# Kernel tuning notes

Measured on AMD Instinct MI355X. Metric: run time of the kernel, lower is better.

## Reference

```python
import jax, jax.numpy as jnp
import numpy as np

V, D, H, L, S_MAX = 32000, 1024, 16, 4, 1024
HD = D // H          # head dim = 64
FF = 4 * D           # mlp hidden = 4096
B, S = 2, 1024


def _layernorm(x, w, b, eps=1e-5):
    mu = jnp.mean(x, axis=-1, keepdims=True)
    var = jnp.mean(jnp.square(x - mu), axis=-1, keepdims=True)
    return (x - mu) * jax.lax.rsqrt(var + eps) * w + b


def setup_inputs() -> dict:
    key = jax.random.key(0)
    ks = jax.random.split(key, 16)
    r = lambda k, shape: (jax.random.normal(k, shape, dtype=jnp.float32) * 0.02)
    return {
        "input_ids": jax.random.randint(ks[0], (B, S), 0, V),
        "tok_emb": r(ks[1], (V, D)),
        "pos_emb": r(ks[2], (S_MAX, D)),
        "ln1_w": jnp.ones((L, D)), "ln1_b": jnp.zeros((L, D)),
        "ln2_w": jnp.ones((L, D)), "ln2_b": jnp.zeros((L, D)),
        "q_w": r(ks[3], (L, D, D)), "q_b": jnp.zeros((L, D)),
        "k_w": r(ks[4], (L, D, D)), "k_b": jnp.zeros((L, D)),
        "v_w": r(ks[5], (L, D, D)), "v_b": jnp.zeros((L, D)),
        "o_w": r(ks[6], (L, D, D)), "o_b": jnp.zeros((L, D)),
        "fc1_w": r(ks[7], (L, FF, D)), "fc1_b": jnp.zeros((L, FF)),
        "fc2_w": r(ks[8], (L, D, FF)), "fc2_b": jnp.zeros((L, D)),
        "lnf_w": jnp.ones((D,)), "lnf_b": jnp.zeros((D,)),
        "head_w": r(ks[9], (V, D)),
    }


def reference(input_ids, tok_emb, pos_emb, ln1_w, ln1_b, ln2_w, ln2_b,
              q_w, q_b, k_w, k_b, v_w, v_b, o_w, o_b,
              fc1_w, fc1_b, fc2_w, fc2_b, lnf_w, lnf_b, head_w):
    b, s = input_ids.shape
    x = tok_emb[input_ids] + pos_emb[:s][None, :, :]          # [B,S,D]
    causal = jnp.tril(jnp.ones((s, s), dtype=bool))           # [S,S]
    scale = 1.0 / np.sqrt(HD)
    for i in range(L):
        # --- causal MHA block ---
        h = _layernorm(x, ln1_w[i], ln1_b[i])
        q = (h @ q_w[i].T + q_b[i]).reshape(b, s, H, HD)
        k = (h @ k_w[i].T + k_b[i]).reshape(b, s, H, HD)
        v = (h @ v_w[i].T + v_b[i]).reshape(b, s, H, HD)
        scores = jnp.einsum('bqhd,bkhd->bhqk', q, k) * scale  # [B,H,S,S]
        scores = jnp.where(causal[None, None], scores, -jnp.inf)
        attn = jax.nn.softmax(scores, axis=-1)
        y = jnp.einsum('bhqk,bkhd->bqhd', attn, v).reshape(b, s, D)
        x = x + (y @ o_w[i].T + o_b[i])
        # --- GELU MLP block (exact gelu, matching torch F.gelu default) ---
        h = _layernorm(x, ln2_w[i], ln2_b[i])
        h = jax.nn.gelu(h @ fc1_w[i].T + fc1_b[i], approximate=False)
        x = x + (h @ fc2_w[i].T + fc2_b[i])
    x = _layernorm(x, lnf_w, lnf_b)
    logits = x[:, -1, :] @ head_w.T                           # [B,V]
    return logits
```

## Files before the change

### kernel.cpp

```cpp
#include <hip/hip_runtime.h>

#define V_SIZE 32000
#define D_DIM  1024
#define H_HEADS 16
#define L_LAYERS 4
#define HD_DIM 64
#define FF_DIM 4096
#define B_BATCH 2
#define S_SEQ  1024
#define M_ROWS (B_BATCH*S_SEQ)
#define KSPL   2

typedef short  s16x8 __attribute__((ext_vector_type(8)));
typedef unsigned short u16x8 __attribute__((ext_vector_type(8)));
typedef float  f32x4 __attribute__((ext_vector_type(4)));
typedef unsigned short u16;
typedef unsigned int   u32;

__device__ inline u16 f2bf(float f){
    u32 u = __float_as_uint(f);
    return (u16)((u + 0x7FFFu + ((u >> 16) & 1u)) >> 16);
}
__device__ inline float b2f(u32 v){ return __uint_as_float(v << 16); }

__device__ inline float gelu_f(float v){
    float y = 0.7978845608f * (v + 0.044715f*v*v*v);
    y = fmaxf(-15.f, fminf(15.f, y));
    float u = __expf(-2.f*y);
    return v / (1.f + u);
}

__device__ inline char* lds_swz(void* base, int row, int byteoff){
    return (char*)base + row*128 + (byteoff ^ ((row & 7) << 4));
}

__device__ inline void gload16(const u16* g, u16* l){
    __builtin_amdgcn_global_load_lds(
        (const __attribute__((address_space(1))) void*)g,
        (__attribute__((address_space(3))) void*)l, 16, 0, 0);
}

__device__ inline int swz_src_col(int lin){
    int row = lin >> 3, s8 = lin & 7;
    return (s8*8) ^ ((row & 7) << 3);
}

__global__ __launch_bounds__(256) void cvt_all_k(
    const float* __restrict__ qw, const float* __restrict__ kw,
    const float* __restrict__ vw, const float* __restrict__ ow,
    const float* __restrict__ f1w, const float* __restrict__ f2w,
    u16* __restrict__ w_qkv, u16* __restrict__ w_o,
    u16* __restrict__ w_f1, u16* __restrict__ w_f2)
{
    const long M1 = 1L << 20;
    const int bx = blockIdx.x;
    const float* s; u16* d; long base;
    if (bx < 3072){
        int which = bx >> 10;
        s = (which==0) ? qw : ((which==1) ? kw : vw);
        base = (long)(bx & 1023) * 4096;
        long layer = base >> 20, rem = base & (M1 - 1);
        d = w_qkv + layer*3*M1 + which*M1 + rem;
        s += base;
    } else if (bx < 4096){
        base = (long)(bx - 3072) * 4096; s = ow  + base; d = w_o  + base;
    } else if (bx < 8192){
        base = (long)(bx - 4096) * 4096; s = f1w + base; d = w_f1 + base;
    } else {
        base = (long)(bx - 8192) * 4096; s = f2w + base; d = w_f2 + base;
    }
    const int t4 = threadIdx.x * 4;
#pragma unroll
    for (int j = 0; j < 4; j++){
        float4 v = *(const float4*)(s + j*1024 + t4);
        uint2 pk;
        pk.x = (u32)f2bf(v.x) | ((u32)f2bf(v.y) << 16);
        pk.y = (u32)f2bf(v.z) | ((u32)f2bf(v.w) << 16);
        *(uint2*)(d + j*1024 + t4) = pk;
    }
}

__global__ __launch_bounds__(256) void embed_ln_k(
    const int* __restrict__ ids, const float* __restrict__ tok,
    const float* __restrict__ pos, const float* __restrict__ lw,
    const float* __restrict__ lb, float* __restrict__ x, u16* __restrict__ h)
{
    int row = blockIdx.x;
    int id  = ids[row];
    int s   = row & (S_SEQ - 1);
    int t   = threadIdx.x;
    float4 tv = *(const float4*)(tok + (size_t)id * D_DIM + t*4);
    float4 pv = *(const float4*)(pos + (size_t)s  * D_DIM + t*4);
    float4 vv;
    vv.x = tv.x + pv.x; vv.y = tv.y + pv.y; vv.z = tv.z + pv.z; vv.w = tv.w + pv.w;
    *(float4*)(x + (size_t)row * D_DIM + t*4) = vv;
    float sm  = vv.x + vv.y + vv.z + vv.w;
    float ss = vv.x*vv.x + vv.y*vv.y + vv.z*vv.z + vv.w*vv.w;
#pragma unroll
    for (int off = 1; off < 64; off <<= 1){
        sm += __shfl_xor(sm, off);
        ss += __shfl_xor(ss, off);
    }
    __shared__ float red[8];
    const int wid = t >> 6, lane = t & 63;
    if (lane == 0){ red[wid] = sm; red[4 + wid] = ss; }
    __syncthreads();
    sm = red[0] + red[1] + red[2] + red[3];
    ss = red[4] + red[5] + red[6] + red[7];
    float mu   = sm * (1.0f/1024.0f);
    float rstd = rsqrtf(ss * (1.0f/1024.0f) - mu*mu + 1e-5f);
    float4 wv = *(const float4*)(lw + t*4);
    float4 bv = *(const float4*)(lb + t*4);
    uint2 pk;
    pk.x = (u32)f2bf((vv.x-mu)*rstd*wv.x + bv.x) | ((u32)f2bf((vv.y-mu)*rstd*wv.y + bv.y) << 16);
    pk.y = (u32)f2bf((vv.z-mu)*rstd*wv.z + bv.z) | ((u32)f2bf((vv.w-mu)*rstd*wv.w + bv.w) << 16);
    *(uint2*)(h + (size_t)row * D_DIM + t*4) = pk;
}

__global__ __launch_bounds__(256) void layernorm_f_k(
    const float* __restrict__ x, const float* __restrict__ w, const float* __restrict__ bb,
    float* __restrict__ outF)
{
    const int row = blockIdx.x * S_SEQ + S_SEQ - 1;
    const int t = threadIdx.x;
    float4 vv = *(const float4*)(x + (size_t)row * D_DIM + t*4);
    float s  = vv.x + vv.y + vv.z + vv.w;
    float ss = vv.x*vv.x + vv.y*vv.y + vv.z*vv.z + vv.w*vv.w;
#pragma unroll
    for (int off = 1; off < 64; off <<= 1){
        s  += __shfl_xor(s,  off);
        ss += __shfl_xor(ss, off);
    }
    __shared__ float red[8];
    const int wid = t >> 6, lane = t & 63;
    if (lane == 0){ red[wid] = s; red[4 + wid] = ss; }
    __syncthreads();
    s  = red[0] + red[1] + red[2] + red[3];
    ss = red[4] + red[5] + red[6] + red[7];
    float mu   = s * (1.0f/1024.0f);
    float rstd = rsqrtf(ss * (1.0f/1024.0f) - mu*mu + 1e-5f);
    float4 wv = *(const float4*)(w  + t*4);
    float4 bv = *(const float4*)(bb + t*4);
    float4 o;
    o.x = (vv.x - mu)*rstd*wv.x + bv.x;
    o.y = (vv.y - mu)*rstd*wv.y + bv.y;
    o.z = (vv.z - mu)*rstd*wv.z + bv.z;
    o.w = (vv.w - mu)*rstd*wv.w + bv.w;
    *(float4*)(outF + (size_t)blockIdx.x * D_DIM + t*4) = o;
}

template<int DOLN>
__global__ __launch_bounds__(256) void reduce_ln_k(
    const u16* __restrict__ part, const float* __restrict__ bias,
    float* __restrict__ x,
    const float* __restrict__ lw, const float* __restrict__ lb,
    u16* __restrict__ h)
{
    const int row = blockIdx.x, t = threadIdx.x;
    const size_t off = (size_t)row * D_DIM + t*4;
    float4 a = *(float4*)(x + off);
    float4 bv = *(const float4*)(bias + t*4);
    a.x += bv.x; a.y += bv.y; a.z += bv.z; a.w += bv.w;
#pragma unroll
    for (int si = 0; si < KSPL; si++){
        uint2 pv = *(const uint2*)(part + (size_t)si * M_ROWS * D_DIM + off);
        a.x += b2f(pv.x & 0xffffu); a.y += b2f(pv.x >> 16);
        a.z += b2f(pv.y & 0xffffu); a.w += b2f(pv.y >> 16);
    }
    *(float4*)(x + off) = a;
    if (DOLN){
        float sm = a.x + a.y + a.z + a.w;
        float ss = a.x*a.x + a.y*a.y + a.z*a.z + a.w*a.w;
#pragma unroll
        for (int o2 = 1; o2 < 64; o2 <<= 1){
            sm += __shfl_xor(sm, o2);
            ss += __shfl_xor(ss, o2);
        }
        __shared__ float red[8];
        const int wid = t >> 6, lane = t & 63;
        if (lane == 0){ red[wid] = sm; red[4 + wid] = ss; }
        __syncthreads();
        sm = red[0] + red[1] + red[2] + red[3];
        ss = red[4] + red[5] + red[6] + red[7];
        float mu   = sm * (1.0f/1024.0f);
        float rstd = rsqrtf(ss * (1.0f/1024.0f) - mu*mu + 1e-5f);
        float4 wv = *(const float4*)(lw + t*4);
        float4 lbv = *(const float4*)(lb + t*4);
        uint2 pk;
        pk.x = (u32)f2bf((a.x-mu)*rstd*wv.x + lbv.x) | ((u32)f2bf((a.y-mu)*rstd*wv.y + lbv.y) << 16);
        pk.y = (u32)f2bf((a.z-mu)*rstd*wv.z + lbv.z) | ((u32)f2bf((a.w-mu)*rstd*wv.w + lbv.w) << 16);
        *(uint2*)(h + (size_t)row * D_DIM + t*4) = pk;
    }
}

__global__ __launch_bounds__(256) void gemm_fc1_k(
    const u16* __restrict__ A, const u16* __restrict__ Bw,
    const float* __restrict__ b0, u16* __restrict__ outB, int Ndim, int Kdim)
{
    const int nx = gridDim.x, ny = gridDim.y;
    const int nwg = nx*ny;
    int orig = blockIdx.y*nx + blockIdx.x;
    int wg = (orig & 7)*(nwg >> 3) + (orig >> 3);
    const int bm = wg % nx;
    const int bn = wg / nx;

    const int nk = Kdim >> 6;

    __shared__ __align__(16) u16 As[2][128*64];
    __shared__ __align__(16) u16 Bs[2][128*64];

    const int t = threadIdx.x;
    const int wid = t >> 6, lane = t & 63, lr = lane & 15, lg = lane >> 4;
    const int wr = wid >> 1, wc = wid & 1;

    f32x4 acc[4][4];
#pragma unroll
    for (int m=0;m<4;m++)
#pragma unroll
        for (int n=0;n<4;n++) acc[m][n] = (f32x4){0.f,0.f,0.f,0.f};

    const u16* Abase = A  + (size_t)(bm*128)*Kdim;
    const u16* Bbase = Bw + (size_t)(bn*128)*Kdim;

    auto stage = [&](int koff, int buf){
#pragma unroll
        for (int i=0;i<4;i++){
            int lin = i*256 + t;
            int row = lin >> 3;
            int sc  = swz_src_col(lin);
            gload16(Abase + (size_t)row*Kdim + koff + sc, &As[buf][lin*8]);
        }
#pragma unroll
        for (int i=0;i<4;i++){
            int lin = i*256 + t;
            int row = lin >> 3;
            int sc  = swz_src_col(lin);
            gload16(Bbase + (size_t)row*Kdim + koff + sc, &Bs[buf][lin*8]);
        }
    };

    stage(0, 0);
    __syncthreads();
    int cb = 0;
    for (int ki = 0; ki < nk; ki++){
        if (ki+1 < nk) stage((ki+1)*64, cb^1);
#pragma unroll
        for (int kk=0;kk<2;kk++){
            s16x8 a[4], b[4];
#pragma unroll
            for (int m=0;m<4;m++)
                a[m] = *(s16x8*)lds_swz(As[cb], wr*64 + m*16 + lr, kk*64 + lg*16);
#pragma unroll
            for (int n=0;n<4;n++)
                b[n] = *(s16x8*)lds_swz(Bs[cb], wc*64 + n*16 + lr, kk*64 + lg*16);
#pragma unroll
            for (int m=0;m<4;m++)
#pragma unroll
                for (int n=0;n<4;n++)
                    acc[m][n] = __builtin_amdgcn_mfma_f32_16x16x32_bf16(a[m], b[n], acc[m][n], 0, 0, 0);
        }
        __syncthreads();
        cb ^= 1;
    }

#pragma unroll
    for (int n=0;n<4;n++){
        int col = bn*128 + wc*64 + n*16 + lr;
        float bvv = b0[col];
#pragma unroll
        for (int m=0;m<4;m++){
            int row0 = bm*128 + wr*64 + m*16 + lg*4;
#pragma unroll
            for (int j=0;j<4;j++){
                int row = row0 + j;
                float val = gelu_f(acc[m][n][j] + bvv);
                outB[(size_t)row * Ndim + col] = f2bf(val);
            }
        }
    }
}

__global__ __launch_bounds__(256) void gemm_qkv_k(
    const u16* __restrict__ A, const u16* __restrict__ Bw,
    const float* __restrict__ b0, const float* __restrict__ b1, const float* __restrict__ b2,
    u16* __restrict__ outB, int Ndim, int Kdim)
{
    const int nx = gridDim.x, ny = gridDim.y;
    const int nwg = nx*ny;
    int orig = blockIdx.y*nx + blockIdx.x;
    int wg = (orig & 7)*(nwg >> 3) + (orig >> 3);
    const int bm = wg % nx;
    const int bn = wg / nx;
    const int nk = Kdim >> 6;

    __shared__ __align__(16) u16 As[2][64*64];
    __shared__ __align__(16) u16 Bs[2][128*64];

    const int t = threadIdx.x;
    const int wid = t >> 6, lane = t & 63, lr = lane & 15, lg = lane >> 4;
    const int wr = wid >> 1, wc = wid & 1;

    f32x4 acc[2][4];
#pragma unroll
    for (int m=0;m<2;m++)
#pragma unroll
        for (int n=0;n<4;n++) acc[m][n] = (f32x4){0.f,0.f,0.f,0.f};

    const u16* Abase = A  + (size_t)(bm*64)*Kdim;
    const u16* Bbase = Bw + (size_t)(bn*128)*Kdim;

    auto stage = [&](int koff, int buf){
#pragma unroll
        for (int i=0;i<2;i++){
            int lin = i*256 + t;
            int row = lin >> 3;
            int sc  = swz_src_col(lin);
            gload16(Abase + (size_t)row*Kdim + koff + sc, &As[buf][lin*8]);
        }
#pragma unroll
        for (int i=0;i<4;i++){
            int lin = i*256 + t;
            int row = lin >> 3;
            int sc  = swz_src_col(lin);
            gload16(Bbase + (size_t)row*Kdim + koff + sc, &Bs[buf][lin*8]);
        }
    };

    stage(0, 0);
    __syncthreads();
    int cb = 0;
    for (int ki = 0; ki < nk; ki++){
        if (ki+1 < nk) stage((ki+1)*64, cb^1);
#pragma unroll
        for (int kk=0;kk<2;kk++){
            s16x8 a[2], b[4];
#pragma unroll
            for (int m=0;m<2;m++)
                a[m] = *(s16x8*)lds_swz(As[cb], wr*32 + m*16 + lr, kk*64 + lg*16);
#pragma unroll
            for (int n=0;n<4;n++)
                b[n] = *(s16x8*)lds_swz(Bs[cb], wc*64 + n*16 + lr, kk*64 + lg*16);
#pragma unroll
            for (int m=0;m<2;m++)
#pragma unroll
                for (int n=0;n<4;n++)
                    acc[m][n] = __builtin_amdgcn_mfma_f32_16x16x32_bf16(a[m], b[n], acc[m][n], 0, 0, 0);
        }
        __syncthreads();
        cb ^= 1;
    }

#pragma unroll
    for (int n=0;n<4;n++){
        int col = bn*128 + wc*64 + n*16 + lr;
        int which = col >> 10;
        const float* bp = (which==0) ? b0 : ((which==1) ? b1 : b2);
        float bvv = bp[col & 1023];
        float scl = (which == 0) ? 0.125f : 1.0f;
#pragma unroll
        for (int m=0;m<2;m++){
            int row0 = bm*64 + wr*32 + m*16 + lg*4;
#pragma unroll
            for (int j=0;j<4;j++){
                int row = row0 + j;
                float val = (acc[m][n][j] + bvv) * scl;
                outB[(size_t)row * Ndim + col] = f2bf(val);
            }
        }
    }
}

__global__ __launch_bounds__(256) void gemm64_k(
    const u16* __restrict__ A, const u16* __restrict__ Bw,
    u16* __restrict__ outP, int Ndim, int Kdim, int kper)
{
    const int nx = gridDim.x, ny = gridDim.y;
    const int nwg = nx*ny*gridDim.z;
    int orig = (blockIdx.z*ny + blockIdx.y)*nx + blockIdx.x;
    int wg = (orig & 7)*(nwg >> 3) + (orig >> 3);
    const int bm = wg % nx; wg /= nx;
    const int bn = wg % ny;
    const int z  = wg / ny;
    const int kbeg = z * kper;
    const int nk = kper >> 6;

    __shared__ __align__(16) u16 As[2][64*64];
    __shared__ __align__(16) u16 Bs[2][128*64];

    const int t = threadIdx.x;
    const int wid = t >> 6, lane = t & 63, lr = lane & 15, lg = lane >> 4;
    const int wr = wid >> 1, wc = wid & 1;

    f32x4 acc[2][4];
#pragma unroll
    for (int m=0;m<2;m++)
#pragma unroll
        for (int n=0;n<4;n++) acc[m][n] = (f32x4){0.f,0.f,0.f,0.f};

    const u16* Abase = A  + (size_t)(bm*64)*Kdim + kbeg;
    const u16* Bbase = Bw + (size_t)(bn*128)*Kdim + kbeg;

    auto stage = [&](int koff, int buf){
#pragma unroll
        for (int i=0;i<2;i++){
            int lin = i*256 + t;
            int row = lin >> 3;
            int sc  = swz_src_col(lin);
            gload16(Abase + (size_t)row*Kdim + koff + sc, &As[buf][lin*8]);
        }
#pragma unroll
        for (int i=0;i<4;i++){
            int lin = i*256 + t;
            int row = lin >> 3;
            int sc  = swz_src_col(lin);
            gload16(Bbase + (size_t)row*Kdim + koff + sc, &Bs[buf][lin*8]);
        }
    };

    stage(0, 0);
    __syncthreads();
    int cb = 0;
    for (int ki = 0; ki < nk; ki++){
        if (ki+1 < nk) stage((ki+1)*64, cb^1);
#pragma unroll
        for (int kk=0;kk<2;kk++){
            s16x8 a[2], b[4];
#pragma unroll
            for (int m=0;m<2;m++)
                a[m] = *(s16x8*)lds_swz(As[cb], wr*32 + m*16 + lr, kk*64 + lg*16);
#pragma unroll
            for (int n=0;n<4;n++)
                b[n] = *(s16x8*)lds_swz(Bs[cb], wc*64 + n*16 + lr, kk*64 + lg*16);
#pragma unroll
            for (int m=0;m<2;m++)
#pragma unroll
                for (int n=0;n<4;n++)
                    acc[m][n] = __builtin_amdgcn_mfma_f32_16x16x32_bf16(a[m], b[n], acc[m][n], 0, 0, 0);
        }
        __syncthreads();
        cb ^= 1;
    }

#pragma unroll
    for (int n=0;n<4;n++){
        int col = bn*128 + wc*64 + n*16 + lr;
#pragma unroll
        for (int m=0;m<2;m++){
            int row0 = bm*64 + wr*32 + m*16 + lg*4;
#pragma unroll
            for (int j=0;j<4;j++){
                int row = row0 + j;
                outP[(size_t)z * M_ROWS * Ndim + (size_t)row * Ndim + col] = f2bf(acc[m][n][j]);
            }
        }
    }
}

__global__ __launch_bounds__(256) void attn_k(
    const u16* __restrict__ qkv, u16* __restrict__ y)
{
    const int gx = gridDim.x;
    const int nwg = gx * gridDim.y;
    int orig = blockIdx.y*gx + blockIdx.x;
    int wg = (orig & 7)*(nwg >> 3) + (orig >> 3);
    const int p  = wg % gx;
    const int bh = wg / gx;
    const int b  = bh >> 4, h = bh & 15;

    const int s_lo = p, s_hi = 15 - p;
    const int ntiles = s_hi + 1;

    __shared__ __align__(16) u16 Ks[2][64*64];
    __shared__ __align__(16) u16 VTs[2][64*64];
    __shared__ __align__(16) u16 Ps[4][16*64];

    const int t = threadIdx.x, wid = t >> 6, lane = t & 63, lr = lane & 15, lg = lane >> 4;
    const size_t rowb = (size_t)b * S_SEQ;
    const u16* qp = qkv + h*HD_DIM;
    const u16* kp = qkv + 1024 + h*HD_DIM;
    const u16* vp = qkv + 2048 + h*HD_DIM;

    const int qw_lo = s_lo*64 + wid*16;
    const int qw_hi = s_hi*64 + wid*16;

    s16x8 aq_lo[2], aq_hi[2];
#pragma unroll
    for (int kc=0;kc<2;kc++){
        aq_lo[kc] = *(const s16x8*)(qp + (rowb + qw_lo + lr) * 3072 + kc*32 + lg*8);
        aq_hi[kc] = *(const s16x8*)(qp + (rowb + qw_hi + lr) * 3072 + kc*32 + lg*8);
    }

    f32x4 o_lo[4], o_hi[4];
#pragma unroll
    for (int n=0;n<4;n++){ o_lo[n] = (f32x4){0.f,0.f,0.f,0.f}; o_hi[n] = (f32x4){0.f,0.f,0.f,0.f}; }
    float l_lo[4] = {0.f,0.f,0.f,0.f}, l_hi[4] = {0.f,0.f,0.f,0.f};

    const int kpr = t >> 3, dsl = t & 7;
    u16x8 vr0, vr1;

    auto issueK = [&](int kt, int buf){
#pragma unroll
        for (int i=0;i<2;i++){
            int lin = i*256 + t;
            int row = lin >> 3;
            int sc  = swz_src_col(lin);
            gload16(kp + (rowb + kt*64 + row)*3072 + sc, &Ks[buf][lin*8]);
        }
    };
    auto loadV = [&](int kt){
        vr0 = *(const u16x8*)(vp + (rowb + kt*64 + 2*kpr    )*3072 + dsl*8);
        vr1 = *(const u16x8*)(vp + (rowb + kt*64 + 2*kpr + 1)*3072 + dsl*8);
    };
    auto writeVT = [&](int buf){
#pragma unroll
        for (int j=0;j<8;j++){
            u32 pk = (u32)vr0[j] | ((u32)vr1[j] << 16);
            *(u32*)lds_swz(VTs[buf], dsl*8 + j, kpr*4) = pk;
        }
    };

    auto doStrip = [&](const s16x8* aq, f32x4* o, float* lsum, int qwS, int kt, bool diag, int cb){
        f32x4 sf[4];
#pragma unroll
        for (int n=0;n<4;n++) sf[n] = (f32x4){0.f,0.f,0.f,0.f};
        __builtin_amdgcn_s_setprio(1);
#pragma unroll
        for (int kc=0;kc<2;kc++){
#pragma unroll
            for (int n=0;n<4;n++){
                s16x8 bk = *(s16x8*)lds_swz(Ks[cb], n*16 + lr, kc*64 + lg*16);
                sf[n] = __builtin_amdgcn_mfma_f32_16x16x32_bf16(aq[kc], bk, sf[n], 0, 0, 0);
            }
        }
        __builtin_amdgcn_s_setprio(0);
        float rs[4] = {0.f,0.f,0.f,0.f};
#pragma unroll
        for (int n=0;n<4;n++){
            int key = kt*64 + n*16 + lr;
#pragma unroll
            for (int j=0;j<4;j++){
                float pe = __expf(sf[n][j]);
                if (diag && key > qwS + lg*4 + j) pe = 0.f;
                sf[n][j] = pe; rs[j] += pe;
            }
        }
#pragma unroll
        for (int off=1; off<16; off<<=1){
#pragma unroll
            for (int j=0;j<4;j++) rs[j] += __shfl_xor(rs[j], off);
        }
#pragma unroll
        for (int j=0;j<4;j++) lsum[j] += rs[j];
        u16* Pw = Ps[wid];
#pragma unroll
        for (int n=0;n<4;n++)
#pragma unroll
            for (int j=0;j<4;j++)
                *(u16*)lds_swz(Pw, lg*4 + j, (n*16 + lr)*2) = f2bf(sf[n][j]);
        __builtin_amdgcn_s_setprio(1);
#pragma unroll
        for (int kc=0;kc<2;kc++){
            s16x8 pa = *(s16x8*)lds_swz(Pw, lr, kc*64 + lg*16);
#pragma unroll
            for (int n=0;n<4;n++){
                s16x8 bv = *(s16x8*)lds_swz(VTs[cb], n*16 + lr, kc*64 + lg*16);
                o[n] = __builtin_amdgcn_mfma_f32_16x16x32_bf16(pa, bv, o[n], 0, 0, 0);
            }
        }
        __builtin_amdgcn_s_setprio(0);
    };

    issueK(0, 0); loadV(0); writeVT(0);
    __syncthreads();
    int cb = 0;
    for (int kt = 0; kt < ntiles; kt++){
        const bool more = (kt+1 < ntiles);
        if (more){ issueK(kt+1, cb^1); loadV(kt+1); }

        doStrip(aq_hi, o_hi, l_hi, qw_hi, kt, kt == s_hi, cb);
        if (kt <= s_lo)
            doStrip(aq_lo, o_lo, l_lo, qw_lo, kt, kt == s_lo, cb);

        if (more) writeVT(cb^1);
        __syncthreads();
        cb ^= 1;
    }

    float inv_lo[4], inv_hi[4];
#pragma unroll
    for (int j=0;j<4;j++){ inv_lo[j] = 1.0f / l_lo[j]; inv_hi[j] = 1.0f / l_hi[j]; }
#pragma unroll
    for (int n=0;n<4;n++)
#pragma unroll
        for (int j=0;j<4;j++){
            y[(rowb + qw_hi + lg*4 + j) * D_DIM + h*HD_DIM + n*16 + lr] = f2bf(o_hi[n][j] * inv_hi[j]);
            y[(rowb + qw_lo + lg*4 + j) * D_DIM + h*HD_DIM + n*16 + lr] = f2bf(o_lo[n][j] * inv_lo[j]);
        }
}

__global__ __launch_bounds__(256) void head_k(
    const float* __restrict__ xf, const float* __restrict__ hw, float* __restrict__ out)
{
    __shared__ float xs[2*D_DIM];
    int t = threadIdx.x;
#pragma unroll
    for (int i=0;i<2;i++){
        int j = t + i*256;
        *(float4*)&xs[j*4] = *(const float4*)(xf + j*4);
    }
    __syncthreads();
    int wid = t >> 6, lane = t & 63;
    int vrow = blockIdx.x * 4 + wid;
    float s0 = 0.f, s1 = 0.f;
#pragma unroll
    for (int it=0; it<4; it++){
        int j = it*64 + lane;
        float4 w4 = *(const float4*)(hw + (size_t)vrow * D_DIM + j*4);
        float4 x0 = *(const float4*)&xs[j*4];
        float4 x1 = *(const float4*)&xs[D_DIM + j*4];
        s0 += w4.x*x0.x + w4.y*x0.y + w4.z*x0.z + w4.w*x0.w;
        s1 += w4.x*x1.x + w4.y*x1.y + w4.z*x1.z + w4.w*x1.w;
    }
#pragma unroll
    for (int off=1; off<64; off<<=1){
        s0 += __shfl_xor(s0, off);
        s1 += __shfl_xor(s1, off);
    }
    if (lane == 0){
        out[vrow]          = s0;
        out[V_SIZE + vrow] = s1;
    }
}

extern "C" void kernel_launch(void* const* d_in, const int* in_sizes, int n_in,
                              void* d_out, int out_size, void* d_ws, size_t ws_size,
                              hipStream_t stream)
{
    (void)in_sizes; (void)n_in; (void)out_size; (void)ws_size;
    const int*   ids  = (const int*)  d_in[0];
    const float* tok  = (const float*)d_in[1];
    const float* pos  = (const float*)d_in[2];
    const float* ln1w = (const float*)d_in[3];
    const float* ln1b = (const float*)d_in[4];
    const float* ln2w = (const float*)d_in[5];
    const float* ln2b = (const float*)d_in[6];
    const float* qw   = (const float*)d_in[7];
    const float* qbi  = (const float*)d_in[8];
    const float* kw   = (const float*)d_in[9];
    const float* kbi  = (const float*)d_in[10];
    const float* vw   = (const float*)d_in[11];
    const float* vbi  = (const float*)d_in[12];
    const float* ow   = (const float*)d_in[13];
    const float* obi  = (const float*)d_in[14];
    const float* f1w  = (const float*)d_in[15];
    const float* f1b  = (const float*)d_in[16];
    const float* f2w  = (const float*)d_in[17];
    const float* f2b  = (const float*)d_in[18];
    const float* lnfw = (const float*)d_in[19];
    const float* lnfb = (const float*)d_in[20];
    const float* hw   = (const float*)d_in[21];

    const long MD = (long)1024*1024;
    char* p = (char*)d_ws;
    float* x    = (float*)p; p += (size_t)M_ROWS * D_DIM * 4;
    u16* h      = (u16*)p;   p += (size_t)M_ROWS * D_DIM * 2;
    u16* qkvbuf = (u16*)p;   p += (size_t)M_ROWS * 3072 * 2;
    u16* ybuf   = (u16*)p;   p += (size_t)M_ROWS * D_DIM * 2;
    u16* h1     = (u16*)p;   p += (size_t)M_ROWS * FF_DIM * 2;
    u16* part   = (u16*)p;   p += (size_t)KSPL * M_ROWS * D_DIM * 2;
    u16* wbuf   = (u16*)p;   p += (size_t)48 * MD * 2;
    float* xf   = (float*)p; p += (size_t)2 * D_DIM * 4;
    float* logits = (float*)d_out;

    u16* w_qkv = wbuf;
    u16* w_o   = wbuf + 12*MD;
    u16* w_f1  = wbuf + 16*MD;
    u16* w_f2  = wbuf + 32*MD;

    cvt_all_k<<<dim3(12288), 256, 0, stream>>>(
        qw, kw, vw, ow, f1w, f2w, w_qkv, w_o, w_f1, w_f2);

    embed_ln_k<<<dim3(M_ROWS), 256, 0, stream>>>(ids, tok, pos, ln1w, ln1b, x, h);

    for (int i = 0; i < L_LAYERS; i++){
        gemm_qkv_k<<<dim3(32, 24), 256, 0, stream>>>(
            h, w_qkv + (size_t)i*3*MD,
            qbi + i*D_DIM, kbi + i*D_DIM, vbi + i*D_DIM,
            qkvbuf, 3072, D_DIM);
        attn_k<<<dim3(8, 32), 256, 0, stream>>>(qkvbuf, ybuf);
        gemm64_k<<<dim3(32, 8, KSPL), 256, 0, stream>>>(
            ybuf, w_o + (size_t)i*MD, part, D_DIM, D_DIM, D_DIM/KSPL);
        reduce_ln_k<1><<<dim3(M_ROWS), 256, 0, stream>>>(
            part, obi + i*D_DIM, x, ln2w + i*D_DIM, ln2b + i*D_DIM, h);
        gemm_fc1_k<<<dim3(16, 32), 256, 0, stream>>>(
            h, w_f1 + (size_t)i*4*MD, f1b + i*FF_DIM, h1, FF_DIM, D_DIM);
        gemm64_k<<<dim3(32, 8, KSPL), 256, 0, stream>>>(
            h1, w_f2 + (size_t)i*4*MD, part, D_DIM, FF_DIM, FF_DIM/KSPL);
        if (i < L_LAYERS-1){
            reduce_ln_k<1><<<dim3(M_ROWS), 256, 0, stream>>>(
                part, f2b + i*D_DIM, x, ln1w + (i+1)*D_DIM, ln1b + (i+1)*D_DIM, h);
        } else {
            reduce_ln_k<0><<<dim3(M_ROWS), 256, 0, stream>>>(
                part, f2b + i*D_DIM, x, nullptr, nullptr, nullptr);
        }
    }

    layernorm_f_k<<<dim3(B_BATCH), 256, 0, stream>>>(x, lnfw, lnfb, xf);
    head_k<<<dim3(V_SIZE/4), 256, 0, stream>>>(xf, hw, logits);
}
```

Measured before the change: 612.6 us.

## Compute only last-token rows in final layer after QKV projection

```diff
diff --git a/kernel.cpp b/kernel.cpp
--- a/kernel.cpp
+++ b/kernel.cpp
@@ -43,6 +43,15 @@
 __device__ inline int swz_src_col(int lin){
     int row = lin >> 3, s8 = lin & 7;
     return (s8*8) ^ ((row & 7) << 3);
+}
+
+__device__ inline s16x8 cvt8(float4 a, float4 b){
+    s16x8 o;
+    o[0]=(short)f2bf(a.x); o[1]=(short)f2bf(a.y);
+    o[2]=(short)f2bf(a.z); o[3]=(short)f2bf(a.w);
+    o[4]=(short)f2bf(b.x); o[5]=(short)f2bf(b.y);
+    o[6]=(short)f2bf(b.z); o[7]=(short)f2bf(b.w);
+    return o;
 }
 
 __global__ __launch_bounds__(256) void cvt_all_k(
@@ -69,14 +78,13 @@
     } else {
         base = (long)(bx - 8192) * 4096; s = f2w + base; d = w_f2 + base;
     }
-    const int t4 = threadIdx.x * 4;
-#pragma unroll
-    for (int j = 0; j < 4; j++){
-        float4 v = *(const float4*)(s + j*1024 + t4);
-        uint2 pk;
-        pk.x = (u32)f2bf(v.x) | ((u32)f2bf(v.y) << 16);
-        pk.y = (u32)f2bf(v.z) | ((u32)f2bf(v.w) << 16);
-        *(uint2*)(d + j*1024 + t4) = pk;
+    const int t8 = threadIdx.x * 8;
+#pragma unroll
+    for (int j = 0; j < 2; j++){
+        const float* sp = s + j*2048 + t8;
+        float4 v0 = *(const float4*)(sp);
+        float4 v1 = *(const float4*)(sp + 4);
+        *(s16x8*)(d + j*2048 + t8) = cvt8(v0, v1);
     }
 }
 
@@ -117,13 +125,41 @@
     *(uint2*)(h + (size_t)row * D_DIM + t*4) = pk;
 }
 
-__global__ __launch_bounds__(256) void layernorm_f_k(
-    const float* __restrict__ x, const float* __restrict__ w, const float* __restrict__ bb,
+__global__ __launch_bounds__(256) void ln_k(
+    const float* __restrict__ x, const float* __restrict__ lw,
+    const float* __restrict__ lb, u16* __restrict__ h)
+{
+    const int row = blockIdx.x, t = threadIdx.x;
+    float4 a = *(const float4*)(x + (size_t)row * D_DIM + t*4);
+    float sm = a.x + a.y + a.z + a.w;
+    float ss = a.x*a.x + a.y*a.y + a.z*a.z + a.w*a.w;
+#pragma unroll
+    for (int o2 = 1; o2 < 64; o2 <<= 1){
+        sm += __shfl_xor(sm, o2);
+        ss += __shfl_xor(ss, o2);
+    }
+    __shared__ float red[8];
+    const int wid = t >> 6, lane = t & 63;
+    if (lane == 0){ red[wid] = sm; red[4 + wid] = ss; }
+    __syncthreads();
+    sm = red[0] + red[1] + red[2] + red[3];
+    ss = red[4] + red[5] + red[6] + red[7];
+    float mu   = sm * (1.0f/1024.0f);
+    float rstd = rsqrtf(ss * (1.0f/1024.0f) - mu*mu + 1e-5f);
+    float4 wv  = *(const float4*)(lw + t*4);
+    float4 lbv = *(const float4*)(lb + t*4);
+    uint2 pk;
+    pk.x = (u32)f2bf((a.x-mu)*rstd*wv.x + lbv.x) | ((u32)f2bf((a.y-mu)*rstd*wv.y + lbv.y) << 16);
+    pk.y = (u32)f2bf((a.z-mu)*rstd*wv.z + lbv.z) | ((u32)f2bf((a.w-mu)*rstd*wv.w + lbv.w) << 16);
+    *(uint2*)(h + (size_t)row * D_DIM + t*4) = pk;
+}
+
+__global__ __launch_bounds__(256) void ln_pair_f_k(
+    const float* __restrict__ x2, const float* __restrict__ w, const float* __restrict__ bb,
     float* __restrict__ outF)
 {
-    const int row = blockIdx.x * S_SEQ + S_SEQ - 1;
-    const int t = threadIdx.x;
-    float4 vv = *(const float4*)(x + (size_t)row * D_DIM + t*4);
+    const int row = blockIdx.x, t = threadIdx.x;
+    float4 vv = *(const float4*)(x2 + (size_t)row * D_DIM + t*4);
     float s  = vv.x + vv.y + vv.z + vv.w;
     float ss = vv.x*vv.x + vv.y*vv.y + vv.z*vv.z + vv.w*vv.w;
 #pragma unroll
@@ -146,10 +182,9 @@
     o.y = (vv.y - mu)*rstd*wv.y + bv.y;
     o.z = (vv.z - mu)*rstd*wv.z + bv.z;
     o.w = (vv.w - mu)*rstd*wv.w + bv.w;
-    *(float4*)(outF + (size_t)blockIdx.x * D_DIM + t*4) = o;
-}
-
-template<int DOLN>
+    *(float4*)(outF + (size_t)row * D_DIM + t*4) = o;
+}
+
 __global__ __launch_bounds__(256) void reduce_ln_k(
     const u16* __restrict__ part, const float* __restrict__ bias,
     float* __restrict__ x,
@@ -168,29 +203,27 @@
         a.z += b2f(pv.y & 0xffffu); a.w += b2f(pv.y >> 16);
     }
     *(float4*)(x + off) = a;
-    if (DOLN){
-        float sm = a.x + a.y + a.z + a.w;
-        float ss = a.x*a.x + a.y*a.y + a.z*a.z + a.w*a.w;
-#pragma unroll
-        for (int o2 = 1; o2 < 64; o2 <<= 1){
-            sm += __shfl_xor(sm, o2);
-            ss += __shfl_xor(ss, o2);
-        }
-        __shared__ float red[8];
-        const int wid = t >> 6, lane = t & 63;
-        if (lane == 0){ red[wid] = sm; red[4 + wid] = ss; }
-        __syncthreads();
-        sm = red[0] + red[1] + red[2] + red[3];
-        ss = red[4] + red[5] + red[6] + red[7];
-        float mu   = sm * (1.0f/1024.0f);
-        float rstd = rsqrtf(ss * (1.0f/1024.0f) - mu*mu + 1e-5f);
-        float4 wv = *(const float4*)(lw + t*4);
-        float4 lbv = *(const float4*)(lb + t*4);
-        uint2 pk;
-        pk.x = (u32)f2bf((a.x-mu)*rstd*wv.x + lbv.x) | ((u32)f2bf((a.y-mu)*rstd*wv.y + lbv.y) << 16);
-        pk.y = (u32)f2bf((a.z-mu)*rstd*wv.z + lbv.z) | ((u32)f2bf((a.w-mu)*rstd*wv.w + lbv.w) << 16);
-        *(uint2*)(h + (size_t)row * D_DIM + t*4) = pk;
-    }
+    float sm = a.x + a.y + a.z + a.w;
+    float ss = a.x*a.x + a.y*a.y + a.z*a.z + a.w*a.w;
+#pragma unroll
+    for (int o2 = 1; o2 < 64; o2 <<= 1){
+        sm += __shfl_xor(sm, o2);
+        ss += __shfl_xor(ss, o2);
+    }
+    __shared__ float red[8];
+    const int wid = t >> 6, lane = t & 63;
+    if (lane == 0){ red[wid] = sm; red[4 + wid] = ss; }
+    __syncthreads();
+    sm = red[0] + red[1] + red[2] + red[3];
+    ss = red[4] + red[5] + red[6] + red[7];
+    float mu   = sm * (1.0f/1024.0f);
+    float rstd = rsqrtf(ss * (1.0f/1024.0f) - mu*mu + 1e-5f);
+    float4 wv = *(const float4*)(lw + t*4);
+    float4 lbv = *(const float4*)(lb + t*4);
+    uint2 pk;
+    pk.x = (u32)f2bf((a.x-mu)*rstd*wv.x + lbv.x) | ((u32)f2bf((a.y-mu)*rstd*wv.y + lbv.y) << 16);
+    pk.y = (u32)f2bf((a.z-mu)*rstd*wv.z + lbv.z) | ((u32)f2bf((a.w-mu)*rstd*wv.w + lbv.w) << 16);
+    *(uint2*)(h + (size_t)row * D_DIM + t*4) = pk;
 }
 
 __global__ __launch_bounds__(256) void gemm_fc1_k(
@@ -596,6 +629,107 @@
             y[(rowb + qw_hi + lg*4 + j) * D_DIM + h*HD_DIM + n*16 + lr] = f2bf(o_hi[n][j] * inv_hi[j]);
             y[(rowb + qw_lo + lg*4 + j) * D_DIM + h*HD_DIM + n*16 + lr] = f2bf(o_lo[n][j] * inv_lo[j]);
         }
+}
+
+__global__ __launch_bounds__(256) void attn_last_k(
+    const u16* __restrict__ qkv, float* __restrict__ Yp, float* __restrict__ psp)
+{
+    const int chunk = blockIdx.x;
+    const int bh = blockIdx.y;
+    const int b = bh >> 4, h = bh & 15;
+    const int t = threadIdx.x;
+    const size_t rowb = (size_t)b * S_SEQ;
+    const size_t qrow = rowb + S_SEQ - 1;
+    __shared__ float qs[64];
+    __shared__ float ps[256];
+    __shared__ float red[4];
+    __shared__ float yred[4][64];
+    if (t < 64) qs[t] = b2f(qkv[qrow*3072 + h*HD_DIM + t]);
+    __syncthreads();
+    int k = chunk*256 + t;
+    const u16* krow = qkv + (rowb + k)*3072 + 1024 + h*HD_DIM;
+    float s = 0.f;
+#pragma unroll
+    for (int j=0;j<8;j++){
+        u16x8 kv = *(const u16x8*)(krow + j*8);
+#pragma unroll
+        for (int e=0;e<8;e++) s += qs[j*8+e] * b2f((u32)(unsigned short)kv[e]);
+    }
+    float p = __expf(s);
+    ps[t] = p;
+    float sp_ = p;
+#pragma unroll
+    for (int off=1; off<64; off<<=1) sp_ += __shfl_xor(sp_, off);
+    if ((t & 63) == 0) red[t>>6] = sp_;
+    __syncthreads();
+    if (t == 0) psp[chunk*32 + bh] = red[0]+red[1]+red[2]+red[3];
+    int d = t & 63, c = t >> 6;
+    float acc = 0.f;
+    const u16* vbase = qkv + (rowb + chunk*256 + c*64)*3072 + 2048 + h*HD_DIM + d;
+    for (int kk=0; kk<64; kk++)
+        acc += ps[c*64 + kk] * b2f((u32)vbase[(size_t)kk*3072]);
+    yred[c][d] = acc;
+    __syncthreads();
+    if (t < 64)
+        Yp[(chunk*32 + bh)*64 + t] = yred[0][t]+yred[1][t]+yred[2][t]+yred[3][t];
+}
+
+__global__ __launch_bounds__(64) void attn_comb_k(
+    const float* __restrict__ Yp, const float* __restrict__ psp, u16* __restrict__ y2)
+{
+    int bh = blockIdx.x, t = threadIdx.x;
+    float psum = psp[bh] + psp[32+bh] + psp[64+bh] + psp[96+bh];
+    float y = Yp[bh*64+t] + Yp[(32+bh)*64+t] + Yp[(64+bh)*64+t] + Yp[(96+bh)*64+t];
+    int b = bh >> 4, h = bh & 15;
+    y2[b*1024 + h*64 + t] = f2bf(y / psum);
+}
+
+template<int MODE>
+__global__ __launch_bounds__(256) void rowpair_k(
+    const u16* __restrict__ A2, const u16* __restrict__ W,
+    const float* __restrict__ bias, const float* __restrict__ xin,
+    float* __restrict__ outF, u16* __restrict__ outB,
+    int Ndim, int Kdim)
+{
+    const int t = threadIdx.x, wid = t >> 6, lane = t & 63;
+    const int colsPerBlock = Ndim >> 8;
+    const int colsPerWave  = colsPerBlock >> 2;
+    const int nj = Kdim >> 9;
+    for (int cc = 0; cc < colsPerWave; cc++){
+        int col = blockIdx.x * colsPerBlock + wid * colsPerWave + cc;
+        const u16* wrow = W + (size_t)col * Kdim;
+        float s0 = 0.f, s1 = 0.f;
+        for (int j = 0; j < nj; j++){
+            int k = j*512 + lane*8;
+            u16x8 wv = *(const u16x8*)(wrow + k);
+            u16x8 a0 = *(const u16x8*)(A2 + k);
+            u16x8 a1 = *(const u16x8*)(A2 + Kdim + k);
+#pragma unroll
+            for (int e=0;e<8;e++){
+                float wf = b2f((u32)wv[e]);
+                s0 += b2f((u32)a0[e]) * wf;
+                s1 += b2f((u32)a1[e]) * wf;
+            }
+        }
+#pragma unroll
+        for (int off=1; off<64; off<<=1){
+            s0 += __shfl_xor(s0, off);
+            s1 += __shfl_xor(s1, off);
+        }
+        if (lane == 0){
+            float bv = bias[col];
+            if (MODE == 0){
+                outF[col]         = xin[(size_t)(S_SEQ-1)*D_DIM + col]   + bv + s0;
+                outF[D_DIM + col] = xin[(size_t)(2*S_SEQ-1)*D_DIM + col] + bv + s1;
+            } else if (MODE == 1){
+                outB[col]         = f2bf(gelu_f(s0 + bv));
+                outB[Ndim + col]  = f2bf(gelu_f(s1 + bv));
+            } else {
+                outF[col]         = xin[col]         + bv + s0;
+                outF[D_DIM + col] = xin[D_DIM + col] + bv + s1;
+            }
+        }
+    }
 }
 
 __global__ __launch_bounds__(256) void head_k(
@@ -669,7 +803,14 @@
     u16* h1     = (u16*)p;   p += (size_t)M_ROWS * FF_DIM * 2;
     u16* part   = (u16*)p;   p += (size_t)KSPL * M_ROWS * D_DIM * 2;
     u16* wbuf   = (u16*)p;   p += (size_t)48 * MD * 2;
-    float* xf   = (float*)p; p += (size_t)2 * D_DIM * 4;
+    float* xf   = (float*)p; p += 2 * D_DIM * 4;
+    u16*   y2   = (u16*)p;   p += 2 * D_DIM * 2;
+    float* x2   = (float*)p; p += 2 * D_DIM * 4;
+    float* x3   = (float*)p; p += 2 * D_DIM * 4;
+    u16*   h2   = (u16*)p;   p += 2 * D_DIM * 2;
+    u16*   g2   = (u16*)p;   p += 2 * FF_DIM * 2;
+    float* Yp   = (float*)p; p += 4 * 32 * 64 * 4;
+    float* psp  = (float*)p; p += 4 * 32 * 4;
     float* logits = (float*)d_out;
 
     u16* w_qkv = wbuf;
@@ -682,7 +823,7 @@
 
     embed_ln_k<<<dim3(M_ROWS), 256, 0, stream>>>(ids, tok, pos, ln1w, ln1b, x, h);
 
-    for (int i = 0; i < L_LAYERS; i++){
+    for (int i = 0; i < L_LAYERS - 1; i++){
         gemm_qkv_k<<<dim3(32, 24), 256, 0, stream>>>(
             h, w_qkv + (size_t)i*3*MD,
             qbi + i*D_DIM, kbi + i*D_DIM, vbi + i*D_DIM,
@@ -690,21 +831,31 @@
         attn_k<<<dim3(8, 32), 256, 0, stream>>>(qkvbuf, ybuf);
         gemm64_k<<<dim3(32, 8, KSPL), 256, 0, stream>>>(
             ybuf, w_o + (size_t)i*MD, part, D_DIM, D_DIM, D_DIM/KSPL);
-        reduce_ln_k<1><<<dim3(M_ROWS), 256, 0, stream>>>(
+        reduce_ln_k<<<dim3(M_ROWS), 256, 0, stream>>>(
             part, obi + i*D_DIM, x, ln2w + i*D_DIM, ln2b + i*D_DIM, h);
         gemm_fc1_k<<<dim3(16, 32), 256, 0, stream>>>(
             h, w_f1 + (size_t)i*4*MD, f1b + i*FF_DIM, h1, FF_DIM, D_DIM);
         gemm64_k<<<dim3(32, 8, KSPL), 256, 0, stream>>>(
             h1, w_f2 + (size_t)i*4*MD, part, D_DIM, FF_DIM, FF_DIM/KSPL);
-        if (i < L_LAYERS-1){
-            reduce_ln_k<1><<<dim3(M_ROWS), 256, 0, stream>>>(
-                part, f2b + i*D_DIM, x, ln1w + (i+1)*D_DIM, ln1b + (i+1)*D_DIM, h);
-        } else {
-            reduce_ln_k<0><<<dim3(M_ROWS), 256, 0, stream>>>(
-                part, f2b + i*D_DIM, x, nullptr, nullptr, nullptr);
-        }
-    }
-
-    layernorm_f_k<<<dim3(B_BATCH), 256, 0, stream>>>(x, lnfw, lnfb, xf);
+        reduce_ln_k<<<dim3(M_ROWS), 256, 0, stream>>>(
+            part, f2b + i*D_DIM, x, ln1w + (i+1)*D_DIM, ln1b + (i+1)*D_DIM, h);
+    }
+
+    const int L3 = L_LAYERS - 1;
+    gemm_qkv_k<<<dim3(32, 24), 256, 0, stream>>>(
+        h, w_qkv + (size_t)L3*3*MD,
+        qbi + L3*D_DIM, kbi + L3*D_DIM, vbi + L3*D_DIM,
+        qkvbuf, 3072, D_DIM);
+    attn_last_k<<<dim3(4, 32), 256, 0, stream>>>(qkvbuf, Yp, psp);
+    attn_comb_k<<<dim3(32), 64, 0, stream>>>(Yp, psp, y2);
+    rowpair_k<0><<<dim3(256), 256, 0, stream>>>(
+        y2, w_o + (size_t)L3*MD, obi + L3*D_DIM, x, x2, nullptr, D_DIM, D_DIM);
+    ln_k<<<dim3(2), 256, 0, stream>>>(x2, ln2w + L3*D_DIM, ln2b + L3*D_DIM, h2);
+    rowpair_k<1><<<dim3(256), 256, 0, stream>>>(
+        h2, w_f1 + (size_t)L3*4*MD, f1b + L3*FF_DIM, nullptr, nullptr, g2, FF_DIM, D_DIM);
+    rowpair_k<2><<<dim3(256), 256, 0, stream>>>(
+        g2, w_f2 + (size_t)L3*4*MD, f2b + L3*D_DIM, x2, x3, nullptr, D_DIM, FF_DIM);
+    ln_pair_f_k<<<dim3(2), 256, 0, stream>>>(x3, lnfw, lnfb, xf);
+
     head_k<<<dim3(V_SIZE/4), 256, 0, stream>>>(xf, hw, logits);
 }
```

Result: faster. 533.6 us (-12.9%).
